# Kernel tuning notes

Measured on AMD Instinct MI355X. Metric: run time of the kernel, lower is better.

The kernel has to match this reference:

```python
import jax, jax.numpy as jnp
import numpy as np

BATCH, T, N_STATE, N_IN, N_OUT = 256, 4096, 32, 8, 8
DT = 1e-3


def setup_inputs() -> dict:
    key = jax.random.key(0)
    k_u, k_x0, k_A, k_B, k_C, k_D = jax.random.split(key, 6)
    t = jnp.arange(T, dtype=jnp.float32) * DT
    u = jax.random.normal(k_u, (BATCH, T, N_IN), dtype=jnp.float32)
    x0 = jax.random.normal(k_x0, (BATCH, N_STATE), dtype=jnp.float32)
    # Stable-ish LTI system parameters
    A = (0.1 / np.sqrt(N_STATE)) * jax.random.normal(k_A, (N_STATE, N_STATE), dtype=jnp.float32) - 0.5 * jnp.eye(N_STATE, dtype=jnp.float32)
    B = jax.random.normal(k_B, (N_STATE, N_IN), dtype=jnp.float32) / np.sqrt(N_IN)
    C = jax.random.normal(k_C, (N_OUT, N_STATE), dtype=jnp.float32) / np.sqrt(N_STATE)
    D = jax.random.normal(k_D, (N_OUT, N_IN), dtype=jnp.float32) / np.sqrt(N_IN)
    return {"t": t, "u": u, "x0": x0, "A": A, "B": B, "C": C, "D": D}


def _dopri5_solve(t, u, x0, A, B):
    """Fixed-step Dopri5 (Dormand-Prince 5th order) on a uniform grid.

    Mirrors diffrax.diffeqsolve(Dopri5, ConstantStepSize, dt0=t[1], saveat=ts=t):
    one RK step per grid interval. u is evaluated at stage times via linear
    interpolation between grid samples.
    """
    dt = t[1] - t[0]

    def f(x, uu):  # vector field: dx = A x + B u
        return x @ A.T + uu @ B.T

    ut = jnp.swapaxes(u, 0, 1)  # [T, BATCH, N_IN]

    def step(x, uu):
        u0, u1 = uu
        du = u1 - u0
        k1 = f(x, u0)
        k2 = f(x + dt * (0.2 * k1), u0 + 0.2 * du)
        k3 = f(x + dt * (3.0 / 40.0 * k1 + 9.0 / 40.0 * k2), u0 + 0.3 * du)
        k4 = f(x + dt * (44.0 / 45.0 * k1 - 56.0 / 15.0 * k2 + 32.0 / 9.0 * k3), u0 + 0.8 * du)
        k5 = f(x + dt * (19372.0 / 6561.0 * k1 - 25360.0 / 2187.0 * k2 + 64448.0 / 6561.0 * k3 - 212.0 / 729.0 * k4), u0 + (8.0 / 9.0) * du)
        k6 = f(x + dt * (9017.0 / 3168.0 * k1 - 355.0 / 33.0 * k2 + 46732.0 / 5247.0 * k3 + 49.0 / 176.0 * k4 - 5103.0 / 18656.0 * k5), u1)
        xn = x + dt * (35.0 / 384.0 * k1 + 500.0 / 1113.0 * k3 + 125.0 / 192.0 * k4 - 2187.0 / 6784.0 * k5 + 11.0 / 84.0 * k6)
        return xn, xn

    _, xs_rest = jax.lax.scan(step, x0, (ut[:-1], ut[1:]))
    xs = jnp.concatenate([x0[None], xs_rest], axis=0)  # [T, BATCH, N_STATE]
    return jnp.swapaxes(xs, 0, 1)  # [BATCH, T, N_STATE]


def reference(t, u, x0, A, B, C, D):
    xs = _dopri5_solve(t, u, x0, A, B)          # state trajectory [BATCH, T, N_STATE]
    ys = xs @ C.T + u @ D.T                      # output y = C x + D u, [BATCH, T, N_OUT]
    return xs, ys
```

## Files before the change

kernel.cpp:

```cpp
#include <hip/hip_runtime.h>

#define BATCH 256
#define TT 4096
#define NS 32
#define NI 8
#define NO 8
#define LCH 64
#define NCHUNKS 64

#define WS_M  0
#define WS_N0 1024
#define WS_N1 1280
#define WS_ML 1536
#define WS_V  2560
#define WS_S  (2560 + BATCH * NCHUNKS * NS)
#define WS_F  (WS_S + BATCH * NCHUNKS * NS)

__device__ __forceinline__ float dot4(float4 a, float4 b) {
    return a.x * b.x + a.y * b.y + a.z * b.z + a.w * b.w;
}
__device__ __forceinline__ float4 ld4(const float* p) { return *(const float4*)p; }

__global__ __launch_bounds__(256) void k_pre(const float* __restrict__ tarr,
                                             const float* __restrict__ A,
                                             const float* __restrict__ B,
                                             float* __restrict__ ws) {
    __shared__ float sA[NS * NS], sB[NS * NI];
    __shared__ float Ka[6][NS * NS];
    __shared__ float Kb[6][NS * NI];
    __shared__ float Kc[6][NS * NI];
    __shared__ float Sa[NS * NS], Sb[NS * NI], Sc[NS * NI];
    __shared__ float Pq[2][NS * NS];
    __shared__ float Ms[NS * NS];

    const int tid = threadIdx.x;
    const float dt = tarr[1] - tarr[0];

    for (int e = tid; e < NS * NS; e += 256) sA[e] = A[e];
    for (int e = tid; e < NS * NI; e += 256) sB[e] = B[e];
    __syncthreads();
    for (int e = tid; e < NS * NS; e += 256) Ka[0][e] = sA[e];
    for (int e = tid; e < NS * NI; e += 256) { Kb[0][e] = sB[e]; Kc[0][e] = 0.f; }
    __syncthreads();

    const float atab[5][5] = {
        {0.2f, 0.f, 0.f, 0.f, 0.f},
        {3.f / 40.f, 9.f / 40.f, 0.f, 0.f, 0.f},
        {44.f / 45.f, -56.f / 15.f, 32.f / 9.f, 0.f, 0.f},
        {19372.f / 6561.f, -25360.f / 2187.f, 64448.f / 6561.f, -212.f / 729.f, 0.f},
        {9017.f / 3168.f, -355.f / 33.f, 46732.f / 5247.f, 49.f / 176.f, -5103.f / 18656.f}};
    const float ctab[6] = {0.f, 0.2f, 0.3f, 0.8f, 8.f / 9.f, 1.f};

    for (int st = 1; st <= 5; ++st) {
        for (int e = tid; e < NS * NS; e += 256) {
            float acc = 0.f;
            for (int j = 0; j < st; ++j) acc += atab[st - 1][j] * Ka[j][e];
            Sa[e] = acc;
        }
        for (int e = tid; e < NS * NI; e += 256) {
            float ab = 0.f, ac = 0.f;
            for (int j = 0; j < st; ++j) {
                ab += atab[st - 1][j] * Kb[j][e];
                ac += atab[st - 1][j] * Kc[j][e];
            }
            Sb[e] = ab; Sc[e] = ac;
        }
        __syncthreads();
        {
            const int j = tid & 31, ig = tid >> 5;
            for (int r = 0; r < 4; ++r) {
                const int row = ig + 8 * r;
                float acc = 0.f;
                for (int k = 0; k < NS; ++k) acc += sA[row * NS + k] * Sa[k * NS + j];
                Ka[st][row * NS + j] = sA[row * NS + j] + dt * acc;
            }
            const int jb = tid & 7, rb = tid >> 3;
            float ab = 0.f, ac = 0.f;
            for (int k = 0; k < NS; ++k) {
                ab += sA[rb * NS + k] * Sb[k * NI + jb];
                ac += sA[rb * NS + k] * Sc[k * NI + jb];
            }
            Kb[st][rb * NI + jb] = sB[rb * NI + jb] + dt * ab;
            Kc[st][rb * NI + jb] = ctab[st] * sB[rb * NI + jb] + dt * ac;
        }
        __syncthreads();
    }

    const float btab[6] = {35.f / 384.f, 0.f, 500.f / 1113.f, 125.f / 192.f,
                           -2187.f / 6784.f, 11.f / 84.f};
    for (int e = tid; e < NS * NS; e += 256) {
        float acc = 0.f;
        for (int i2 = 0; i2 < 6; ++i2) acc += btab[i2] * Ka[i2][e];
        const float m = dt * acc + (((e / NS) == (e % NS)) ? 1.f : 0.f);
        ws[WS_M + e] = m;
        Pq[0][e] = m;
        Ms[e] = m;
    }
    for (int e = tid; e < NS * NI; e += 256) {
        float ap = 0.f, aq = 0.f;
        for (int i2 = 0; i2 < 6; ++i2) {
            ap += btab[i2] * Kb[i2][e];
            aq += btab[i2] * Kc[i2][e];
        }
        const float P = dt * ap, Q = dt * aq;
        ws[WS_N0 + e] = P - Q;
        ws[WS_N1 + e] = Q;
        Sb[e] = P - Q;
        Sc[e] = Q;
    }
    __syncthreads();

    int cur = 0;
    for (int itq = 0; itq < 6; ++itq) {
        const int j = tid & 31, ig = tid >> 5;
        for (int r = 0; r < 4; ++r) {
            const int row = ig + 8 * r;
            float acc = 0.f;
            for (int k = 0; k < NS; ++k) acc += Pq[cur][row * NS + k] * Pq[cur][k * NS + j];
            Pq[cur ^ 1][row * NS + j] = acc;
        }
        __syncthreads();
        cur ^= 1;
        if (itq == 2)
            for (int e = tid; e < NS * NS; e += 256) Sa[e] = Pq[cur][e];
    }
    for (int e = tid; e < NS * NS; e += 256) ws[WS_ML + e] = Pq[cur][e];

    float* cb = &Ka[0][0];
    const int rr = tid >> 3, mm = tid & 7;

    float mrow[NS], m8row[NS];
#pragma unroll
    for (int kk = 0; kk < NS; ++kk) { mrow[kk] = Ms[rr * NS + kk]; m8row[kk] = Sa[rr * NS + kk]; }

    {
        float acc = 0.f;
#pragma unroll
        for (int kk = 0; kk < NS; ++kk) acc += mrow[kk] * Sc[kk * NI + mm];
        const float h = Sb[tid] + acc;
        cb[tid] = h;
        ws[WS_F + 63 * (NS * NI) + tid] = h;
    }
    __syncthreads();
    for (int i = 1; i < 8; ++i) {
        float acc = 0.f;
#pragma unroll
        for (int kk = 0; kk < NS; ++kk) acc += m8row[kk] * cb[(i - 1) * 256 + kk * NI + mm];
        cb[i * 256 + tid] = acc;
        ws[WS_F + (63 - 8 * i) * (NS * NI) + tid] = acc;
        __syncthreads();
    }
    int pp = 0;
    for (int k = 1; k < 8; ++k) {
        float acc[8];
#pragma unroll
        for (int i = 0; i < 8; ++i) {
            float a = 0.f;
#pragma unroll
            for (int kk = 0; kk < NS; ++kk) a += mrow[kk] * cb[pp * 2048 + i * 256 + kk * NI + mm];
            acc[i] = a;
        }
#pragma unroll
        for (int i = 0; i < 8; ++i) {
            cb[(pp ^ 1) * 2048 + i * 256 + tid] = acc[i];
            ws[WS_F + (63 - 8 * i - k) * (NS * NI) + tid] = acc[i];
        }
        __syncthreads();
        pp ^= 1;
    }
    ws[WS_F + 64 * (NS * NI) + tid] = Sc[tid];
}

__global__ __launch_bounds__(256, 2) void k_phase1(const float* __restrict__ u,
                                                   float* __restrict__ ws) {
    __shared__ float4 sF[64 * 64];

    const int tid = threadIdx.x;

    const float4* Fg = (const float4*)(ws + WS_F);
    for (int idx = tid; idx < 64 * 64; idx += 256) {
        const int j = idx >> 6, q = (idx >> 3) & 7, s = idx & 7;
        sF[idx] = Fg[(j << 6) + (s << 3) + q];
    }
    __syncthreads();

    const int task = blockIdx.x * 4 + (tid >> 6);
    const int c = task % (NCHUNKS - 1), g = task / (NCHUNKS - 1);
    const int l = tid & 63;
    const int beta = l >> 3, s8 = l & 7;
    const int b = g * 8 + beta;
    const int t0 = c * LCH;
    const float* ub = u + ((size_t)b * TT + t0) * NI;

    float4 ua = ld4(ub), uc = ld4(ub + 4);
    float a0 = 0.f, a1 = 0.f, a2 = 0.f, a3 = 0.f;

#pragma unroll 4
    for (int j = 0; j < 64; ++j) {
        const float4 na = ld4(ub + (j + 1) * NI);
        const float4 nb = ld4(ub + (j + 1) * NI + 4);
        const float4* fj = &sF[(j << 6) + s8];
        const float4 f0 = fj[0], f1 = fj[8], f2 = fj[16], f3 = fj[24];
        const float4 f4 = fj[32], f5 = fj[40], f6 = fj[48], f7 = fj[56];
        a0 += dot4(f0, ua) + dot4(f1, uc);
        a1 += dot4(f2, ua) + dot4(f3, uc);
        a2 += dot4(f4, ua) + dot4(f5, uc);
        a3 += dot4(f6, ua) + dot4(f7, uc);
        ua = na; uc = nb;
    }

    const float* Ft = ws + WS_F + 64 * (NS * NI) + 32 * s8;
    a0 += dot4(ld4(Ft), ua) + dot4(ld4(Ft + 4), uc);
    a1 += dot4(ld4(Ft + 8), ua) + dot4(ld4(Ft + 12), uc);
    a2 += dot4(ld4(Ft + 16), ua) + dot4(ld4(Ft + 20), uc);
    a3 += dot4(ld4(Ft + 24), ua) + dot4(ld4(Ft + 28), uc);

    *(float4*)(ws + WS_V + ((size_t)b * NCHUNKS + c) * NS + 4 * s8) =
        make_float4(a0, a1, a2, a3);
}

__global__ __launch_bounds__(64) void k_phase2(const float* __restrict__ x0,
                                               float* __restrict__ ws) {
    const float* ML = ws + WS_ML;
    const float* v = ws + WS_V;
    float* sst = ws + WS_S;
    const int b = blockIdx.x;
    const int l = threadIdx.x, i = l & 31, h = l >> 5;

    float mlr[16];
#pragma unroll
    for (int jj = 0; jj < 16; ++jj) mlr[jj] = ML[i * NS + 16 * h + jj];

    float x = x0[b * NS + i];
    for (int c = 0; c < NCHUNKS; ++c) {
        if (h == 0) sst[((size_t)b * NCHUNKS + c) * NS + i] = x;
        if (c == NCHUNKS - 1) break;
        float p = 0.f;
#pragma unroll
        for (int jj = 0; jj < 16; ++jj) p += mlr[jj] * __shfl(x, 16 * h + jj, 64);
        p += __shfl_xor(p, 32, 64);
        x = p + v[((size_t)b * NCHUNKS + c) * NS + i];
    }
}

__global__ __launch_bounds__(64, 1) void k_phase3(const float* __restrict__ u,
                                                  float* __restrict__ ws,
                                                  float* __restrict__ out,
                                                  const float* __restrict__ Cc,
                                                  const float* __restrict__ Dd) {
    const float* M = ws + WS_M;
    const float* N0 = ws + WS_N0;
    const float* N1 = ws + WS_N1;

    const int task = blockIdx.x;
    const int c = task % NCHUNKS, g = task / NCHUNKS;
    const int l = threadIdx.x;
    const int beta = l >> 3, s8 = l & 7;
    const int b = g * 8 + beta;
    const int src_base = l & 56;

    float4 mq[4][8];
#pragma unroll
    for (int r = 0; r < 4; ++r)
#pragma unroll
        for (int jj = 0; jj < 8; ++jj) mq[r][jj] = ld4(M + (4 * s8 + r) * NS + 4 * jj);

    float4 n0q[4][2], n1q[4][2];
#pragma unroll
    for (int r = 0; r < 4; ++r) {
        n0q[r][0] = ld4(N0 + (4 * s8 + r) * NI);
        n0q[r][1] = ld4(N0 + (4 * s8 + r) * NI + 4);
        n1q[r][0] = ld4(N1 + (4 * s8 + r) * NI);
        n1q[r][1] = ld4(N1 + (4 * s8 + r) * NI + 4);
    }

    float4 cq[8], dq[2];
#pragma unroll
    for (int jj = 0; jj < 8; ++jj) cq[jj] = ld4(Cc + s8 * NS + 4 * jj);
    dq[0] = ld4(Dd + s8 * NI);
    dq[1] = ld4(Dd + s8 * NI + 4);

    const int t0 = c * LCH;
    const float* ub = u + (size_t)b * TT * NI;
    const float* u_last = ub + (size_t)(TT - 1) * NI;
    const float* up = ub + (size_t)t0 * NI;
    float4 u0a = ld4(up), u0b = ld4(up + 4);
    float4 u1a = ld4(up + NI), u1b = ld4(up + NI + 4);
    const float* up2 = up + 2 * NI;

    float4 mine = ld4(ws + WS_S + ((size_t)b * NCHUNKS + c) * NS + 4 * s8);

    float* xp = out + ((size_t)b * TT + t0) * NS + 4 * s8;
    float* yp = out + (size_t)BATCH * TT * NS + ((size_t)b * TT + t0) * NO + s8;

    for (int js = 0; js < LCH; ++js) {
        float4 xq[8];
#pragma unroll
        for (int jj = 0; jj < 8; ++jj) {
            xq[jj].x = __shfl(mine.x, src_base + jj, 64);
            xq[jj].y = __shfl(mine.y, src_base + jj, 64);
            xq[jj].z = __shfl(mine.z, src_base + jj, 64);
            xq[jj].w = __shfl(mine.w, src_base + jj, 64);
        }

        const float* uq = (up2 > u_last) ? u_last : up2;
        const float4 u2a = ld4(uq);
        const float4 u2b = ld4(uq + 4);

        *(float4*)xp = mine;

        float ya = dot4(cq[0], xq[0]) + dot4(cq[1], xq[1]) + dot4(cq[2], xq[2]) + dot4(cq[3], xq[3]);
        float yb = dot4(cq[4], xq[4]) + dot4(cq[5], xq[5]) + dot4(cq[6], xq[6]) + dot4(cq[7], xq[7]);
        ya += dot4(dq[0], u0a);
        yb += dot4(dq[1], u0b);
        *yp = ya + yb;

        if (js < LCH - 1) {
            float w0, w1, w2, w3;
#pragma unroll
            for (int r = 0; r < 4; ++r) {
                const float pn = dot4(n0q[r][0], u0a) + dot4(n0q[r][1], u0b) +
                                 dot4(n1q[r][0], u1a) + dot4(n1q[r][1], u1b);
                const float pe = dot4(mq[r][0], xq[0]) + dot4(mq[r][2], xq[2]) +
                                 dot4(mq[r][4], xq[4]) + dot4(mq[r][6], xq[6]);
                const float po = dot4(mq[r][1], xq[1]) + dot4(mq[r][3], xq[3]) +
                                 dot4(mq[r][5], xq[5]) + dot4(mq[r][7], xq[7]);
                const float w = pn + pe + po;
                if (r == 0) w0 = w; else if (r == 1) w1 = w; else if (r == 2) w2 = w; else w3 = w;
            }
            mine = make_float4(w0, w1, w2, w3);
            u0a = u1a; u0b = u1b;
            u1a = u2a; u1b = u2b;
        }
        xp += NS;
        yp += NO;
        up2 += NI;
    }
}

extern "C" void kernel_launch(void* const* d_in, const int* in_sizes, int n_in,
                              void* d_out, int out_size, void* d_ws, size_t ws_size,
                              hipStream_t stream) {
    const float* t = (const float*)d_in[0];
    const float* u = (const float*)d_in[1];
    const float* x0 = (const float*)d_in[2];
    const float* A = (const float*)d_in[3];
    const float* B = (const float*)d_in[4];
    const float* C = (const float*)d_in[5];
    const float* D = (const float*)d_in[6];
    float* out = (float*)d_out;
    float* ws = (float*)d_ws;

    k_pre<<<dim3(1), dim3(256), 0, stream>>>(t, A, B, ws);
    k_phase1<<<dim3(8 * (NCHUNKS - 1)), dim3(256), 0, stream>>>(u, ws);
    k_phase2<<<dim3(BATCH), dim3(64), 0, stream>>>(x0, ws);
    k_phase3<<<dim3(32 * NCHUNKS), dim3(64), 0, stream>>>(u, ws, out, C, D);
}
```

Measured before the change: 380.6 us.

## Split phase3 state matvec across 4 lanes per row with LDS broadcast

Phase3 now handles 2 batches per wave instead of 8, splitting each 32-wide dot product across 4 lane groups. Partial sums are combined with xor shuffles, and the state vector is broadcast through double-buffered LDS rather than 32 shuffles per step. Fewer registers per lane allow 4 waves per CU, and the grid grows 4x to raise occupancy and parallelism on the serial per-chunk recurrence. The cost is extra reduction shuffles and LDS waits every step, and three quarters of lanes sit idle during stores.

```diff
diff --git a/kernel.cpp b/kernel.cpp
--- a/kernel.cpp
+++ b/kernel.cpp
@@ -20,6 +20,7 @@
     return a.x * b.x + a.y * b.y + a.z * b.z + a.w * b.w;
 }
 __device__ __forceinline__ float4 ld4(const float* p) { return *(const float4*)p; }
+__device__ __forceinline__ float2 ld2(const float* p) { return *(const float2*)p; }
 
 __global__ __launch_bounds__(256) void k_pre(const float* __restrict__ tarr,
                                              const float* __restrict__ A,
@@ -243,7 +244,7 @@
     }
 }
 
-__global__ __launch_bounds__(64, 1) void k_phase3(const float* __restrict__ u,
+__global__ __launch_bounds__(64, 4) void k_phase3(const float* __restrict__ u,
                                                   float* __restrict__ ws,
                                                   float* __restrict__ out,
                                                   const float* __restrict__ Cc,
@@ -255,86 +256,99 @@
     const int task = blockIdx.x;
     const int c = task % NCHUNKS, g = task / NCHUNKS;
     const int l = threadIdx.x;
-    const int beta = l >> 3, s8 = l & 7;
-    const int b = g * 8 + beta;
-    const int src_base = l & 56;
-
-    float4 mq[4][8];
-#pragma unroll
-    for (int r = 0; r < 4; ++r)
-#pragma unroll
-        for (int jj = 0; jj < 8; ++jj) mq[r][jj] = ld4(M + (4 * s8 + r) * NS + 4 * jj);
-
-    float4 n0q[4][2], n1q[4][2];
+    const int beta2 = l >> 5;
+    const int h = (l >> 3) & 3;
+    const int s8 = l & 7;
+    const int b = g * 2 + beta2;
+
+    float4 mq[4][2];
 #pragma unroll
     for (int r = 0; r < 4; ++r) {
-        n0q[r][0] = ld4(N0 + (4 * s8 + r) * NI);
-        n0q[r][1] = ld4(N0 + (4 * s8 + r) * NI + 4);
-        n1q[r][0] = ld4(N1 + (4 * s8 + r) * NI);
-        n1q[r][1] = ld4(N1 + (4 * s8 + r) * NI + 4);
-    }
-
-    float4 cq[8], dq[2];
-#pragma unroll
-    for (int jj = 0; jj < 8; ++jj) cq[jj] = ld4(Cc + s8 * NS + 4 * jj);
-    dq[0] = ld4(Dd + s8 * NI);
-    dq[1] = ld4(Dd + s8 * NI + 4);
+        mq[r][0] = ld4(M + (4 * s8 + r) * NS + 8 * h);
+        mq[r][1] = ld4(M + (4 * s8 + r) * NS + 8 * h + 4);
+    }
+    float2 n0q[4], n1q[4];
+#pragma unroll
+    for (int r = 0; r < 4; ++r) {
+        n0q[r] = ld2(N0 + (4 * s8 + r) * NI + 2 * h);
+        n1q[r] = ld2(N1 + (4 * s8 + r) * NI + 2 * h);
+    }
+    float4 cq[2];
+    cq[0] = ld4(Cc + s8 * NS + 8 * h);
+    cq[1] = ld4(Cc + s8 * NS + 8 * h + 4);
+    const float2 dq = ld2(Dd + s8 * NI + 2 * h);
 
     const int t0 = c * LCH;
     const float* ub = u + (size_t)b * TT * NI;
-    const float* u_last = ub + (size_t)(TT - 1) * NI;
-    const float* up = ub + (size_t)t0 * NI;
-    float4 u0a = ld4(up), u0b = ld4(up + 4);
-    float4 u1a = ld4(up + NI), u1b = ld4(up + NI + 4);
-    const float* up2 = up + 2 * NI;
+    const float* upl = ub + (size_t)t0 * NI + 2 * h;
+    const float* u_lastl = ub + (size_t)(TT - 1) * NI + 2 * h;
+    float2 u0h = ld2(upl);
+    float2 u1h = ld2(upl + NI);
+    const float* upl2 = upl + 2 * NI;
 
     float4 mine = ld4(ws + WS_S + ((size_t)b * NCHUNKS + c) * NS + 4 * s8);
 
     float* xp = out + ((size_t)b * TT + t0) * NS + 4 * s8;
     float* yp = out + (size_t)BATCH * TT * NS + ((size_t)b * TT + t0) * NO + s8;
 
+    __shared__ float4 xb[2][2 * 8];
+
+    if (h == 0) xb[0][beta2 * 8 + s8] = mine;
+    asm volatile("s_waitcnt lgkmcnt(0)" ::: "memory");
+    __builtin_amdgcn_sched_barrier(0);
+
+    int cur = 0;
     for (int js = 0; js < LCH; ++js) {
-        float4 xq[8];
-#pragma unroll
-        for (int jj = 0; jj < 8; ++jj) {
-            xq[jj].x = __shfl(mine.x, src_base + jj, 64);
-            xq[jj].y = __shfl(mine.y, src_base + jj, 64);
-            xq[jj].z = __shfl(mine.z, src_base + jj, 64);
-            xq[jj].w = __shfl(mine.w, src_base + jj, 64);
-        }
-
-        const float* uq = (up2 > u_last) ? u_last : up2;
-        const float4 u2a = ld4(uq);
-        const float4 u2b = ld4(uq + 4);
-
-        *(float4*)xp = mine;
-
-        float ya = dot4(cq[0], xq[0]) + dot4(cq[1], xq[1]) + dot4(cq[2], xq[2]) + dot4(cq[3], xq[3]);
-        float yb = dot4(cq[4], xq[4]) + dot4(cq[5], xq[5]) + dot4(cq[6], xq[6]) + dot4(cq[7], xq[7]);
-        ya += dot4(dq[0], u0a);
-        yb += dot4(dq[1], u0b);
-        *yp = ya + yb;
+        float4 xq0 = xb[cur][beta2 * 8 + 2 * h];
+        float4 xq1 = xb[cur][beta2 * 8 + 2 * h + 1];
+
+        const float* uq = (upl2 > u_lastl) ? u_lastl : upl2;
+        const float2 u2h = ld2(uq);
+
+        float yv = dot4(cq[0], xq0) + dot4(cq[1], xq1) + dq.x * u0h.x + dq.y * u0h.y;
 
         if (js < LCH - 1) {
             float w0, w1, w2, w3;
 #pragma unroll
             for (int r = 0; r < 4; ++r) {
-                const float pn = dot4(n0q[r][0], u0a) + dot4(n0q[r][1], u0b) +
-                                 dot4(n1q[r][0], u1a) + dot4(n1q[r][1], u1b);
-                const float pe = dot4(mq[r][0], xq[0]) + dot4(mq[r][2], xq[2]) +
-                                 dot4(mq[r][4], xq[4]) + dot4(mq[r][6], xq[6]);
-                const float po = dot4(mq[r][1], xq[1]) + dot4(mq[r][3], xq[3]) +
-                                 dot4(mq[r][5], xq[5]) + dot4(mq[r][7], xq[7]);
-                const float w = pn + pe + po;
-                if (r == 0) w0 = w; else if (r == 1) w1 = w; else if (r == 2) w2 = w; else w3 = w;
+                float wv = dot4(mq[r][0], xq0) + dot4(mq[r][1], xq1);
+                wv += n0q[r].x * u0h.x + n0q[r].y * u0h.y +
+                      n1q[r].x * u1h.x + n1q[r].y * u1h.y;
+                if (r == 0) w0 = wv; else if (r == 1) w1 = wv; else if (r == 2) w2 = wv; else w3 = wv;
+            }
+            yv += __shfl_xor(yv, 8, 64);
+            w0 += __shfl_xor(w0, 8, 64);
+            w1 += __shfl_xor(w1, 8, 64);
+            w2 += __shfl_xor(w2, 8, 64);
+            w3 += __shfl_xor(w3, 8, 64);
+            yv += __shfl_xor(yv, 16, 64);
+            w0 += __shfl_xor(w0, 16, 64);
+            w1 += __shfl_xor(w1, 16, 64);
+            w2 += __shfl_xor(w2, 16, 64);
+            w3 += __shfl_xor(w3, 16, 64);
+
+            if (h == 0) {
+                *(float4*)xp = mine;
+                *yp = yv;
             }
             mine = make_float4(w0, w1, w2, w3);
-            u0a = u1a; u0b = u1b;
-            u1a = u2a; u1b = u2b;
-        }
+            if (h == 0) xb[cur ^ 1][beta2 * 8 + s8] = mine;
+            u0h = u1h;
+            u1h = u2h;
+        } else {
+            yv += __shfl_xor(yv, 8, 64);
+            yv += __shfl_xor(yv, 16, 64);
+            if (h == 0) {
+                *(float4*)xp = mine;
+                *yp = yv;
+            }
+        }
+        asm volatile("s_waitcnt lgkmcnt(0)" ::: "memory");
+        __builtin_amdgcn_sched_barrier(0);
+        cur ^= 1;
         xp += NS;
         yp += NO;
-        up2 += NI;
+        upl2 += NI;
     }
 }
 
@@ -354,5 +368,5 @@
     k_pre<<<dim3(1), dim3(256), 0, stream>>>(t, A, B, ws);
     k_phase1<<<dim3(8 * (NCHUNKS - 1)), dim3(256), 0, stream>>>(u, ws);
     k_phase2<<<dim3(BATCH), dim3(64), 0, stream>>>(x0, ws);
-    k_phase3<<<dim3(32 * NCHUNKS), dim3(64), 0, stream>>>(u, ws, out, C, D);
-}
+    k_phase3<<<dim3(128 * NCHUNKS), dim3(64), 0, stream>>>(u, ws, out, C, D);
+}
```

Result: faster. 361.7 us (-5.0%).
